# Performance work log

Hardware: AMD Instinct MI355X
Metric: run time of the kernel (lower is better)

## Reference

```python
import math
import jax, jax.numpy as jnp
import numpy as np

NUM_BUCKETS = 32
MAX_DISTANCE = 128
NUM_HEADS = 16


def _relative_position_bucket_bidirectional(relative_position):
    # encoder (is_decoder=False): split buckets for positive/negative, then log-spaced
    nb = NUM_BUCKETS // 2  # 16
    buckets = (relative_position > 0).astype(jnp.int32) * nb
    rp = jnp.abs(relative_position)
    max_exact = nb // 2  # 8
    is_small = rp < max_exact
    rp_safe = jnp.maximum(rp, 1)  # avoid log(0); masked out by is_small anyway
    large = max_exact + (
        jnp.log(rp_safe.astype(jnp.float32) / max_exact)
        / math.log(MAX_DISTANCE / max_exact)
        * (nb - max_exact)
    ).astype(jnp.int32)
    large = jnp.minimum(large, nb - 1)
    return buckets + jnp.where(is_small, rp, large)


def compute_bias(rel_bias, tgt_len, src_len):
    ctx = jnp.arange(tgt_len)[:, None]
    mem = jnp.arange(src_len)[None, :]
    buckets = _relative_position_bucket_bidirectional(mem - ctx)  # [T,S]
    values = rel_bias[buckets]            # [T,S,H]
    return jnp.transpose(values, (2, 0, 1))[None]  # [1,H,T,S]


def setup_inputs() -> dict:
    key = jax.random.key(0)
    ks = jax.random.split(key, 7)
    B, S, D = 4, 2048, 1024
    s = 1.0 / math.sqrt(D)
    return {
        "query_states": jax.random.normal(ks[0], (B, S, D), jnp.float32),
        "key_value_states": jax.random.normal(ks[1], (B, S, D), jnp.float32),
        "wq": jax.random.normal(ks[2], (D, D), jnp.float32) * s,
        "wk": jax.random.normal(ks[3], (D, D), jnp.float32) * s,
        "wv": jax.random.normal(ks[4], (D, D), jnp.float32) * s,
        "wo": jax.random.normal(ks[5], (D, D), jnp.float32) * s,
        "rel_bias": jax.random.normal(ks[6], (NUM_BUCKETS, NUM_HEADS), jnp.float32),
    }


def reference(query_states, key_value_states, wq, wk, wv, wo, rel_bias):
    B, T, D = query_states.shape
    S = key_value_states.shape[1]
    H = NUM_HEADS
    dh = D // H

    def shape(x, L):
        return jnp.transpose(x.reshape(B, L, H, dh), (0, 2, 1, 3))  # [B,H,L,dh]

    q = shape(query_states @ wq, T)
    k = shape(key_value_states @ wk, S)
    v = shape(key_value_states @ wv, S)

    bias = compute_bias(rel_bias, T, S)                      # [1,H,T,S]
    scores = jnp.einsum("bhtd,bhsd->bhts", q, k) + bias      # no 1/sqrt(d) scaling (T5)
    weights = jax.nn.softmax(scores, axis=-1)
    attn = jnp.einsum("bhts,bhsd->bhtd", weights, v)
    attn = jnp.transpose(attn, (0, 2, 1, 3)).reshape(B, T, D)
    return attn @ wo
```

## Files before the change

kernel.cpp:

```cpp
#include <hip/hip_runtime.h>
#include <hip/hip_bf16.h>
#include <math.h>

typedef __bf16 bf16;
typedef __attribute__((ext_vector_type(8))) __bf16 bf16x8;
typedef __attribute__((ext_vector_type(4))) __bf16 bf16x4;
typedef __attribute__((ext_vector_type(4))) float f32x4;
typedef __attribute__((ext_vector_type(16))) float f32x16;
typedef __attribute__((ext_vector_type(4), aligned(4))) float f32x4u;

#define B_  4
#define S_  2048
#define D_  1024
#define H_  16
#define DH_ 64
#define M_  (B_ * S_)
#define LOG2E 1.44269504088896f

static __device__ __forceinline__ f32x4 mfma16(bf16x8 a, bf16x8 b, f32x4 c) {
  return __builtin_amdgcn_mfma_f32_16x16x32_bf16(a, b, c, 0, 0, 0);
}
static __device__ __forceinline__ f32x16 mfma32(bf16x8 a, bf16x8 b, f32x16 c) {
  return __builtin_amdgcn_mfma_f32_32x32x16_bf16(a, b, c, 0, 0, 0);
}

static __device__ __forceinline__ void gld_lds16(const bf16* g, bf16* l) {
  __builtin_amdgcn_global_load_lds(
      (const __attribute__((address_space(1))) void*)g,
      (__attribute__((address_space(3))) void*)l, 16, 0, 0);
}

static __device__ __forceinline__ unsigned pkbf(float a, float b) {
  union { struct { __bf16 lo, hi; } s; unsigned u; } x;
  x.s.lo = (bf16)a; x.s.hi = (bf16)b;
  return x.u;
}

__global__ __launch_bounds__(256)
void cast2_kernel(const float* __restrict__ a, const float* __restrict__ bsrc,
                  bf16* __restrict__ oa, bf16* __restrict__ ob) {
  const int blk = blockIdx.x;
  const float* in = (blk < 8192) ? a : bsrc;
  bf16* out = (blk < 8192) ? oa : ob;
  size_t i = ((size_t)(blk & 8191) * 256 + threadIdx.x) * 4;
  float4 v = *(const float4*)(in + i);
  bf16x4 o = {(bf16)v.x, (bf16)v.y, (bf16)v.z, (bf16)v.w};
  *(bf16x4*)(out + i) = o;
}

__global__ __launch_bounds__(256)
void transpose_cast4_kernel(const float* __restrict__ w0, const float* __restrict__ w1,
                            const float* __restrict__ w2, const float* __restrict__ w3,
                            bf16* __restrict__ o0, bf16* __restrict__ o1,
                            bf16* __restrict__ o2, bf16* __restrict__ o3) {
  __shared__ float tile[32][33];
  const int z = blockIdx.z;
  const float* in = (z == 0) ? w0 : (z == 1) ? w1 : (z == 2) ? w2 : w3;
  bf16* out = (z == 0) ? o0 : (z == 1) ? o1 : (z == 2) ? o2 : o3;
  int n0 = blockIdx.x * 32, k0 = blockIdx.y * 32;
  int tx = threadIdx.x, ty = threadIdx.y;
#pragma unroll
  for (int j = 0; j < 32; j += 8)
    tile[ty + j][tx] = in[(size_t)(k0 + ty + j) * D_ + n0 + tx];
  __syncthreads();
#pragma unroll
  for (int j = 0; j < 32; j += 8)
    out[(size_t)(n0 + ty + j) * D_ + k0 + tx] = (bf16)tile[tx][ty + j];
}

__global__ __launch_bounds__(256)
void bias_table_kernel(const float* __restrict__ rel_bias, float* __restrict__ tab) {
  int i = blockIdx.x * 256 + threadIdx.x;
  int h = i >> 12, dp = i & 4095;
  int rel = dp - 2047;
  int bucket = (rel > 0) ? 16 : 0;
  int rp = rel < 0 ? -rel : rel;
  if (rp < 8) {
    bucket += rp;
  } else {
    int large = 8 + (int)(2.0f * __log2f((float)rp * 0.125f));
    bucket += (large < 15 ? large : 15);
  }
  tab[i] = rel_bias[bucket * H_ + h] * LOG2E - 64.0f;
}

__global__ __launch_bounds__(256)
void proj_gemm_kernel(const bf16* __restrict__ Xq, const bf16* __restrict__ Xkv,
                      const bf16* __restrict__ Wq, const bf16* __restrict__ Wk,
                      const bf16* __restrict__ Wv,
                      bf16* __restrict__ Qb, bf16* __restrict__ Kb, bf16* __restrict__ Vt) {
  const int K = D_;
  __shared__ bf16 As[128][64];
  __shared__ bf16 Bs[128][64];
  const int bid = blockIdx.x;
  const int xcd = bid & 7, j = bid >> 3;
  const int bx = j & 7;
  const int p = (j >> 3) + xcd * 24;
  const int by = p & 63, z = p >> 6;
  const bf16* A  = (z == 0) ? Xq : Xkv;
  const bf16* Bt = (z == 0) ? Wq : (z == 1) ? Wk : Wv;
  const int tid = threadIdx.x;
  const int brow = by * 128, bcol = bx * 128;
  const int wave = tid >> 6, lane = tid & 63;
  const int wr = (wave >> 1) * 64, wc = (wave & 1) * 64;
  const int lrow = lane & 15, lgrp = lane >> 4;

  f32x4 acc[4][4] = {};

  const int srow8 = tid >> 3;
  const int scol = ((tid & 7) ^ (srow8 & 7)) * 8;
  const bf16* ag = A + (size_t)(brow + srow8) * K + scol;
  const bf16* bg = Bt + (size_t)(bcol + srow8) * K + scol;
  const size_t r32 = (size_t)32 * K;
  bf16* al = &As[0][0] + tid * 8;
  bf16* bl = &Bs[0][0] + tid * 8;

  const int rsw = (lrow & 7) << 4;
  const char* arp = (const char*)&As[0][0];
  const char* brp = (const char*)&Bs[0][0];

  for (int k0 = 0; k0 < K; k0 += 64) {
    __syncthreads();
    gld_lds16(ag + k0,           al);
    gld_lds16(ag + k0 + r32,     al + 2048);
    gld_lds16(ag + k0 + 2 * r32, al + 4096);
    gld_lds16(ag + k0 + 3 * r32, al + 6144);
    gld_lds16(bg + k0,           bl);
    gld_lds16(bg + k0 + r32,     bl + 2048);
    gld_lds16(bg + k0 + 2 * r32, bl + 4096);
    gld_lds16(bg + k0 + 3 * r32, bl + 6144);
    __syncthreads();
#pragma unroll
    for (int kk = 0; kk < 2; ++kk) {
      bf16x8 af[4], bfr[4];
#pragma unroll
      for (int i = 0; i < 4; ++i) {
        af[i]  = *(const bf16x8*)(arp + (wr + i * 16 + lrow) * 128 +
                                  ((kk * 64 + (lgrp << 4)) ^ rsw));
        bfr[i] = *(const bf16x8*)(brp + (wc + i * 16 + lrow) * 128 +
                                  ((kk * 64 + (lgrp << 4)) ^ rsw));
      }
#pragma unroll
      for (int mi = 0; mi < 4; ++mi)
#pragma unroll
        for (int ni = 0; ni < 4; ++ni)
          acc[mi][ni] = mfma16(af[mi], bfr[ni], acc[mi][ni]);
    }
  }

  const float scl = (z == 0) ? LOG2E : 1.0f;
#pragma unroll
  for (int mi = 0; mi < 4; ++mi) {
    const int rowb = brow + wr + mi * 16 + lgrp * 4;
#pragma unroll
    for (int ni = 0; ni < 4; ++ni) {
      const int col = bcol + wc + ni * 16 + lrow;
      const int hh = col >> 6, d = col & (DH_ - 1);
      if (z == 2) {
        const int bb = rowb >> 11, s = rowb & (S_ - 1);
        bf16x4 pk = {(bf16)acc[mi][ni][0], (bf16)acc[mi][ni][1],
                     (bf16)acc[mi][ni][2], (bf16)acc[mi][ni][3]};
        *(bf16x4*)&Vt[((size_t)((bb * H_ + hh) * DH_ + d)) * S_ + s] = pk;
      } else {
#pragma unroll
        for (int r = 0; r < 4; ++r) {
          const float v = acc[mi][ni][r] * scl;
          const int m = rowb + r;
          const int bb = m >> 11, s = m & (S_ - 1);
          if (z == 0)
            Qb[((size_t)((bb * H_ + hh) * S_ + s)) * DH_ + d] = (bf16)v;
          else
            Kb[((size_t)((bb * H_ + hh) * S_ + s)) * DH_ + d] = (bf16)v;
        }
      }
    }
  }
}

__global__ __launch_bounds__(256)
void gemm_out_kernel(const bf16* __restrict__ A, const bf16* __restrict__ Bt,
                     float* __restrict__ Cout) {
  const int K = D_, N = D_;
  __shared__ bf16 As[128][64];
  __shared__ bf16 Bs[128][64];
  const int bid = blockIdx.x;
  const int xcd = bid & 7, j = bid >> 3;
  const int bx = j & 7;
  const int by = (j >> 3) + xcd * 8;
  const int tid = threadIdx.x;
  const int brow = by * 128, bcol = bx * 128;
  const int wave = tid >> 6, lane = tid & 63;
  const int wr = (wave >> 1) * 64, wc = (wave & 1) * 64;
  const int lrow = lane & 15, lgrp = lane >> 4;

  f32x4 acc[4][4] = {};

  const int srow8 = tid >> 3;
  const int scol = ((tid & 7) ^ (srow8 & 7)) * 8;
  const bf16* ag = A + (size_t)(brow + srow8) * K + scol;
  const bf16* bg = Bt + (size_t)(bcol + srow8) * K + scol;
  const size_t r32 = (size_t)32 * K;
  bf16* al = &As[0][0] + tid * 8;
  bf16* bl = &Bs[0][0] + tid * 8;

  const int rsw = (lrow & 7) << 4;
  const char* arp = (const char*)&As[0][0];
  const char* brp = (const char*)&Bs[0][0];

  for (int k0 = 0; k0 < K; k0 += 64) {
    __syncthreads();
    gld_lds16(ag + k0,           al);
    gld_lds16(ag + k0 + r32,     al + 2048);
    gld_lds16(ag + k0 + 2 * r32, al + 4096);
    gld_lds16(ag + k0 + 3 * r32, al + 6144);
    gld_lds16(bg + k0,           bl);
    gld_lds16(bg + k0 + r32,     bl + 2048);
    gld_lds16(bg + k0 + 2 * r32, bl + 4096);
    gld_lds16(bg + k0 + 3 * r32, bl + 6144);
    __syncthreads();
#pragma unroll
    for (int kk = 0; kk < 2; ++kk) {
      bf16x8 af[4], bfr[4];
#pragma unroll
      for (int i = 0; i < 4; ++i) {
        af[i]  = *(const bf16x8*)(arp + (wr + i * 16 + lrow) * 128 +
                                  ((kk * 64 + (lgrp << 4)) ^ rsw));
        bfr[i] = *(const bf16x8*)(brp + (wc + i * 16 + lrow) * 128 +
                                  ((kk * 64 + (lgrp << 4)) ^ rsw));
      }
#pragma unroll
      for (int mi = 0; mi < 4; ++mi)
#pragma unroll
        for (int ni = 0; ni < 4; ++ni)
          acc[mi][ni] = mfma16(af[mi], bfr[ni], acc[mi][ni]);
    }
  }

#pragma unroll
  for (int mi = 0; mi < 4; ++mi) {
    const int rowb = brow + wr + mi * 16 + lgrp * 4;
#pragma unroll
    for (int ni = 0; ni < 4; ++ni) {
      const int col = bcol + wc + ni * 16 + lrow;
#pragma unroll
      for (int r = 0; r < 4; ++r)
        Cout[(size_t)(rowb + r) * N + col] = acc[mi][ni][r];
    }
  }
}

__global__ __launch_bounds__(512, 4)
void attn_kernel(const bf16* __restrict__ Q, const bf16* __restrict__ Kb,
                 const bf16* __restrict__ Vt, const float* __restrict__ tab,
                 bf16* __restrict__ Oa) {
  __shared__ bf16 SB[4][4096];

  const int bid = blockIdx.x;
  const int w = ((bid & 7) << 6) + (bid >> 3);
  const int qt = w & 7, h = (w >> 3) & 15, b = w >> 7;
  const int tid = threadIdx.x;
  const int wave = tid >> 6, lane = tid & 63;
  const int l31 = lane & 31;
  const int hi = lane >> 5;
  const int t = qt * 256 + wave * 32 + l31;

  const bf16* Qp = Q + (size_t)(b * H_ + h) * S_ * DH_;
  const bf16* Kp = Kb + (size_t)(b * H_ + h) * S_ * DH_;
  const bf16* Vp = Vt + (size_t)(b * H_ + h) * DH_ * S_;
  const float* btb = tab + h * 4096 + 2047 - t;

  const int srow = tid >> 4;
  const int colS = (tid & 15) << 4;
  const int scol = colS ^ ((srow & 15) << 4);
  const bf16* ks0 = Kp + (size_t)(srow + 32 * (scol >> 7)) * DH_ + ((scol & 127) >> 1);
  const bf16* vs0 = Vp + (size_t)(srow + 32 * (scol >> 7)) * S_ + ((scol & 127) >> 1);
  bf16* sd = &SB[0][0] + tid * 8;

  const int swz = (l31 & 15) << 4;
  const char* rb = (const char*)&SB[0][0] + l31 * 256;
  const char* ra[4][2];
#pragma unroll
  for (int c = 0; c < 4; ++c)
#pragma unroll
    for (int sub = 0; sub < 2; ++sub)
      ra[c][sub] = rb + ((c * 32 + hi * 16 + sub * 128) ^ swz);

  bf16x8 qf[4];
#pragma unroll
  for (int c = 0; c < 4; ++c)
    qf[c] = *(const bf16x8*)&Qp[(size_t)t * DH_ + c * 16 + hi * 8];

  float l_r = 0.f;
  f32x16 o0 = {}, o1 = {};

  gld_lds16(ks0, sd);
  gld_lds16(vs0, sd + 8192);
  __syncthreads();

#define ATTN_TILE(BUF, S0)                                                        \
  {                                                                               \
    if ((S0) + 64 < S_) {                                                         \
      const int nb = (BUF) ^ 1;                                                   \
      gld_lds16(ks0 + (size_t)((S0) + 64) * DH_, sd + nb * 4096);                 \
      gld_lds16(vs0 + ((S0) + 64), sd + nb * 4096 + 8192);                        \
    }                                                                             \
    f32x16 sc0, sc1;                                                              \
    _Pragma("unroll")                                                             \
    for (int g = 0; g < 4; ++g) {                                                 \
      f32x4u b0 = *(const f32x4u*)(btb + (S0) + 8 * g + 4 * hi);                  \
      f32x4u b1 = *(const f32x4u*)(btb + (S0) + 32 + 8 * g + 4 * hi);             \
      _Pragma("unroll")                                                           \
      for (int v = 0; v < 4; ++v) { sc0[4 * g + v] = b0[v]; sc1[4 * g + v] = b1[v]; } \
    }                                                                             \
    _Pragma("unroll")                                                             \
    for (int c = 0; c < 4; ++c) {                                                 \
      bf16x8 k0 = *(const bf16x8*)(ra[c][0] + (BUF) * 8192);                      \
      bf16x8 k1 = *(const bf16x8*)(ra[c][1] + (BUF) * 8192);                      \
      sc0 = mfma32(k0, qf[c], sc0);                                               \
      sc1 = mfma32(k1, qf[c], sc1);                                               \
    }                                                                             \
    unsigned pw[16];                                                              \
    float q0s = 0.f, q1s = 0.f, q2s = 0.f, q3s = 0.f;                             \
    _Pragma("unroll")                                                             \
    for (int r2 = 0; r2 < 8; ++r2) {                                              \
      float a0 = __builtin_amdgcn_exp2f(sc0[2 * r2]);                             \
      float a1 = __builtin_amdgcn_exp2f(sc0[2 * r2 + 1]);                         \
      float c0 = __builtin_amdgcn_exp2f(sc1[2 * r2]);                             \
      float c1 = __builtin_amdgcn_exp2f(sc1[2 * r2 + 1]);                         \
      q0s += a0; q1s += a1; q2s += c0; q3s += c1;                                 \
      pw[r2] = pkbf(a0, a1);                                                      \
      pw[8 + r2] = pkbf(c0, c1);                                                  \
    }                                                                             \
    l_r += (q0s + q1s) + (q2s + q3s);                                             \
                 \
    unsigned sh[8];                                                               \
    _Pragma("unroll")                                                             \
    for (int g = 0; g < 4; ++g) {                                                 \
      const int base = (g & 1) * 4 + (g >> 1) * 8;                                \
      sh[2 * g]     = __shfl_xor(hi ? pw[base + 0] : pw[base + 2], 32);           \
      sh[2 * g + 1] = __shfl_xor(hi ? pw[base + 1] : pw[base + 3], 32);           \
    }                                                                             \
    _Pragma("unroll")                                                             \
    for (int g = 0; g < 4; ++g) {                                                 \
      const int base = (g & 1) * 4 + (g >> 1) * 8;                                \
      int4 bi = { (int)(hi ? sh[2 * g]     : pw[base + 0]),                       \
                  (int)(hi ? sh[2 * g + 1] : pw[base + 1]),                       \
                  (int)(hi ? pw[base + 2] : sh[2 * g]),                           \
                  (int)(hi ? pw[base + 3] : sh[2 * g + 1]) };                     \
      bf16x8 pb = *(bf16x8*)&bi;                                                  \
      bf16x8 v0 = *(const bf16x8*)(ra[g][0] + 16384 + (BUF) * 8192);              \
      bf16x8 v1 = *(const bf16x8*)(ra[g][1] + 16384 + (BUF) * 8192);              \
      o0 = mfma32(v0, pb, o0);                                                    \
      o1 = mfma32(v1, pb, o1);                                                    \
    }                                                                             \
    __syncthreads();                                                              \
  }

  for (int s0 = 0; s0 < S_; s0 += 128) {
    ATTN_TILE(0, s0)
    ATTN_TILE(1, s0 + 64)
  }
#undef ATTN_TILE

  l_r += __shfl_xor(l_r, 32);
  const float inv = 1.0f / l_r;
  bf16* Ob = Oa + ((size_t)(b * S_ + t)) * D_ + h * DH_;
#pragma unroll
  for (int g = 0; g < 4; ++g) {
    bf16x4 u0 = {(bf16)(o0[4 * g + 0] * inv), (bf16)(o0[4 * g + 1] * inv),
                 (bf16)(o0[4 * g + 2] * inv), (bf16)(o0[4 * g + 3] * inv)};
    *(bf16x4*)&Ob[8 * g + 4 * hi] = u0;
    bf16x4 u1 = {(bf16)(o1[4 * g + 0] * inv), (bf16)(o1[4 * g + 1] * inv),
                 (bf16)(o1[4 * g + 2] * inv), (bf16)(o1[4 * g + 3] * inv)};
    *(bf16x4*)&Ob[32 + 8 * g + 4 * hi] = u1;
  }
}

extern "C" void kernel_launch(void* const* d_in, const int* in_sizes, int n_in,
                              void* d_out, int out_size, void* d_ws, size_t ws_size,
                              hipStream_t stream) {
  const float* Xq   = (const float*)d_in[0];
  const float* Xkv  = (const float*)d_in[1];
  const float* Wq   = (const float*)d_in[2];
  const float* Wk   = (const float*)d_in[3];
  const float* Wv   = (const float*)d_in[4];
  const float* Wo   = (const float*)d_in[5];
  const float* relb = (const float*)d_in[6];
  float* out = (float*)d_out;

  char* ws = (char*)d_ws;
  const size_t SZ_X = (size_t)M_ * D_ * 2;
  const size_t SZ_W = (size_t)D_ * D_ * 2;
  bf16* Xq_b  = (bf16*)(ws);
  bf16* Xkv_b = (bf16*)(ws + SZ_X);
  bf16* Wq_t  = (bf16*)(ws + 2 * SZ_X);
  bf16* Wk_t  = (bf16*)(ws + 2 * SZ_X + SZ_W);
  bf16* Wv_t  = (bf16*)(ws + 2 * SZ_X + 2 * SZ_W);
  bf16* Wo_t  = (bf16*)(ws + 2 * SZ_X + 3 * SZ_W);
  bf16* Qb    = (bf16*)(ws + 2 * SZ_X + 4 * SZ_W);
  bf16* Kbuf  = (bf16*)(ws + 3 * SZ_X + 4 * SZ_W);
  bf16* Vt    = (bf16*)(ws + 4 * SZ_X + 4 * SZ_W);
  bf16* Ab    = (bf16*)(ws + 5 * SZ_X + 4 * SZ_W);
  float* tab  = (float*)(ws + 6 * SZ_X + 4 * SZ_W);

  cast2_kernel<<<16384, 256, 0, stream>>>(Xq, Xkv, Xq_b, Xkv_b);
  transpose_cast4_kernel<<<dim3(32, 32, 4), dim3(32, 8), 0, stream>>>(
      Wq, Wk, Wv, Wo, Wq_t, Wk_t, Wv_t, Wo_t);
  bias_table_kernel<<<256, 256, 0, stream>>>(relb, tab);

  proj_gemm_kernel<<<1536, 256, 0, stream>>>(
      Xq_b, Xkv_b, Wq_t, Wk_t, Wv_t, Qb, Kbuf, Vt);
  attn_kernel<<<512, 512, 0, stream>>>(Qb, Kbuf, Vt, tab, Ab);
  gemm_out_kernel<<<512, 256, 0, stream>>>(Ab, Wo_t, out);
}
```

Baseline: 205.5 us.

## Double-buffer LDS tiles in projection and output GEMMs with prefetch

Both GEMM kernels switch from a single 128x64 LDS tile per operand to two 128x32 buffers, with a 4-way XOR swizzle. The next K-slice is prefetched with global-to-LDS loads while the MFMAs run on the current buffer, which should overlap memory latency with compute. The cost is half as much work per sync (K-step of 32 instead of 64) and the same total LDS footprint, so each k-step does fewer MFMAs between barriers.

```diff
diff --git a/kernel.cpp b/kernel.cpp
--- a/kernel.cpp
+++ b/kernel.cpp
@@ -90,8 +90,8 @@
                       const bf16* __restrict__ Wv,
                       bf16* __restrict__ Qb, bf16* __restrict__ Kb, bf16* __restrict__ Vt) {
   const int K = D_;
-  __shared__ bf16 As[128][64];
-  __shared__ bf16 Bs[128][64];
+  __shared__ bf16 As[2][128][32];
+  __shared__ bf16 Bs[2][128][32];
   const int bid = blockIdx.x;
   const int xcd = bid & 7, j = bid >> 3;
   const int bx = j & 7;
@@ -107,46 +107,50 @@
 
   f32x4 acc[4][4] = {};
 
-  const int srow8 = tid >> 3;
-  const int scol = ((tid & 7) ^ (srow8 & 7)) * 8;
-  const bf16* ag = A + (size_t)(brow + srow8) * K + scol;
-  const bf16* bg = Bt + (size_t)(bcol + srow8) * K + scol;
-  const size_t r32 = (size_t)32 * K;
-  bf16* al = &As[0][0] + tid * 8;
-  bf16* bl = &Bs[0][0] + tid * 8;
-
-  const int rsw = (lrow & 7) << 4;
-  const char* arp = (const char*)&As[0][0];
-  const char* brp = (const char*)&Bs[0][0];
+  const int schunk = ((tid & 3) ^ ((tid >> 2) & 3)) * 8;
+  const bf16* ag = A + (size_t)(brow + (tid >> 2)) * K + schunk;
+  const bf16* bg = Bt + (size_t)(bcol + (tid >> 2)) * K + schunk;
+  const size_t rstep = (size_t)64 * K;
+  bf16* al = &As[0][0][0] + tid * 8;
+  bf16* bl = &Bs[0][0][0] + tid * 8;
+
+  const int rsw = (lrow & 3) << 4;
+  const char* arp = (const char*)&As[0][0][0];
+  const char* brp = (const char*)&Bs[0][0][0];
+
+  gld_lds16(ag, al);           gld_lds16(ag + rstep, al + 2048);
+  gld_lds16(bg, bl);           gld_lds16(bg + rstep, bl + 2048);
+  __syncthreads();
+
+#define PROJ_TILE(BUF, KO)                                                         \
+  {                                                                                \
+    if ((KO) + 32 < K) {                                                           \
+      gld_lds16(ag + (KO) + 32,         al + ((BUF) ^ 1) * 4096);                  \
+      gld_lds16(ag + (KO) + 32 + rstep, al + ((BUF) ^ 1) * 4096 + 2048);           \
+      gld_lds16(bg + (KO) + 32,         bl + ((BUF) ^ 1) * 4096);                  \
+      gld_lds16(bg + (KO) + 32 + rstep, bl + ((BUF) ^ 1) * 4096 + 2048);           \
+    }                                                                              \
+    bf16x8 af[4], bfr[4];                                                          \
+    _Pragma("unroll")                                                              \
+    for (int i = 0; i < 4; ++i) {                                                  \
+      af[i]  = *(const bf16x8*)(arp + (BUF) * 8192 +                               \
+                                (wr + i * 16 + lrow) * 64 + ((lgrp << 4) ^ rsw));  \
+      bfr[i] = *(const bf16x8*)(brp + (BUF) * 8192 +                               \
+                                (wc + i * 16 + lrow) * 64 + ((lgrp << 4) ^ rsw));  \
+    }                                                                              \
+    _Pragma("unroll")                                                              \
+    for (int mi = 0; mi < 4; ++mi)                                                 \
+      _Pragma("unroll")                                                            \
+      for (int ni = 0; ni < 4; ++ni)                                               \
+        acc[mi][ni] = mfma16(af[mi], bfr[ni], acc[mi][ni]);                        \
+    __syncthreads();                                                               \
+  }
 
   for (int k0 = 0; k0 < K; k0 += 64) {
-    __syncthreads();
-    gld_lds16(ag + k0,           al);
-    gld_lds16(ag + k0 + r32,     al + 2048);
-    gld_lds16(ag + k0 + 2 * r32, al + 4096);
-    gld_lds16(ag + k0 + 3 * r32, al + 6144);
-    gld_lds16(bg + k0,           bl);
-    gld_lds16(bg + k0 + r32,     bl + 2048);
-    gld_lds16(bg + k0 + 2 * r32, bl + 4096);
-    gld_lds16(bg + k0 + 3 * r32, bl + 6144);
-    __syncthreads();
-#pragma unroll
-    for (int kk = 0; kk < 2; ++kk) {
-      bf16x8 af[4], bfr[4];
-#pragma unroll
-      for (int i = 0; i < 4; ++i) {
-        af[i]  = *(const bf16x8*)(arp + (wr + i * 16 + lrow) * 128 +
-                                  ((kk * 64 + (lgrp << 4)) ^ rsw));
-        bfr[i] = *(const bf16x8*)(brp + (wc + i * 16 + lrow) * 128 +
-                                  ((kk * 64 + (lgrp << 4)) ^ rsw));
-      }
-#pragma unroll
-      for (int mi = 0; mi < 4; ++mi)
-#pragma unroll
-        for (int ni = 0; ni < 4; ++ni)
-          acc[mi][ni] = mfma16(af[mi], bfr[ni], acc[mi][ni]);
-    }
-  }
+    PROJ_TILE(0, k0)
+    PROJ_TILE(1, k0 + 32)
+  }
+#undef PROJ_TILE
 
   const float scl = (z == 0) ? LOG2E : 1.0f;
 #pragma unroll
@@ -181,8 +185,8 @@
 void gemm_out_kernel(const bf16* __restrict__ A, const bf16* __restrict__ Bt,
                      float* __restrict__ Cout) {
   const int K = D_, N = D_;
-  __shared__ bf16 As[128][64];
-  __shared__ bf16 Bs[128][64];
+  __shared__ bf16 As[2][128][32];
+  __shared__ bf16 Bs[2][128][32];
   const int bid = blockIdx.x;
   const int xcd = bid & 7, j = bid >> 3;
   const int bx = j & 7;
@@ -195,46 +199,50 @@
 
   f32x4 acc[4][4] = {};
 
-  const int srow8 = tid >> 3;
-  const int scol = ((tid & 7) ^ (srow8 & 7)) * 8;
-  const bf16* ag = A + (size_t)(brow + srow8) * K + scol;
-  const bf16* bg = Bt + (size_t)(bcol + srow8) * K + scol;
-  const size_t r32 = (size_t)32 * K;
-  bf16* al = &As[0][0] + tid * 8;
-  bf16* bl = &Bs[0][0] + tid * 8;
-
-  const int rsw = (lrow & 7) << 4;
-  const char* arp = (const char*)&As[0][0];
-  const char* brp = (const char*)&Bs[0][0];
+  const int schunk = ((tid & 3) ^ ((tid >> 2) & 3)) * 8;
+  const bf16* ag = A + (size_t)(brow + (tid >> 2)) * K + schunk;
+  const bf16* bg = Bt + (size_t)(bcol + (tid >> 2)) * K + schunk;
+  const size_t rstep = (size_t)64 * K;
+  bf16* al = &As[0][0][0] + tid * 8;
+  bf16* bl = &Bs[0][0][0] + tid * 8;
+
+  const int rsw = (lrow & 3) << 4;
+  const char* arp = (const char*)&As[0][0][0];
+  const char* brp = (const char*)&Bs[0][0][0];
+
+  gld_lds16(ag, al);           gld_lds16(ag + rstep, al + 2048);
+  gld_lds16(bg, bl);           gld_lds16(bg + rstep, bl + 2048);
+  __syncthreads();
+
+#define OUT_TILE(BUF, KO)                                                          \
+  {                                                                                \
+    if ((KO) + 32 < K) {                                                           \
+      gld_lds16(ag + (KO) + 32,         al + ((BUF) ^ 1) * 4096);                  \
+      gld_lds16(ag + (KO) + 32 + rstep, al + ((BUF) ^ 1) * 4096 + 2048);           \
+      gld_lds16(bg + (KO) + 32,         bl + ((BUF) ^ 1) * 4096);                  \
+      gld_lds16(bg + (KO) + 32 + rstep, bl + ((BUF) ^ 1) * 4096 + 2048);           \
+    }                                                                              \
+    bf16x8 af[4], bfr[4];                                                          \
+    _Pragma("unroll")                                                              \
+    for (int i = 0; i < 4; ++i) {                                                  \
+      af[i]  = *(const bf16x8*)(arp + (BUF) * 8192 +                               \
+                                (wr + i * 16 + lrow) * 64 + ((lgrp << 4) ^ rsw));  \
+      bfr[i] = *(const bf16x8*)(brp + (BUF) * 8192 +                               \
+                                (wc + i * 16 + lrow) * 64 + ((lgrp << 4) ^ rsw));  \
+    }                                                                              \
+    _Pragma("unroll")                                                              \
+    for (int mi = 0; mi < 4; ++mi)                                                 \
+      _Pragma("unroll")                                                            \
+      for (int ni = 0; ni < 4; ++ni)                                               \
+        acc[mi][ni] = mfma16(af[mi], bfr[ni], acc[mi][ni]);                        \
+    __syncthreads();                                                               \
+  }
 
   for (int k0 = 0; k0 < K; k0 += 64) {
-    __syncthreads();
-    gld_lds16(ag + k0,           al);
-    gld_lds16(ag + k0 + r32,     al + 2048);
-    gld_lds16(ag + k0 + 2 * r32, al + 4096);
-    gld_lds16(ag + k0 + 3 * r32, al + 6144);
-    gld_lds16(bg + k0,           bl);
-    gld_lds16(bg + k0 + r32,     bl + 2048);
-    gld_lds16(bg + k0 + 2 * r32, bl + 4096);
-    gld_lds16(bg + k0 + 3 * r32, bl + 6144);
-    __syncthreads();
-#pragma unroll
-    for (int kk = 0; kk < 2; ++kk) {
-      bf16x8 af[4], bfr[4];
-#pragma unroll
-      for (int i = 0; i < 4; ++i) {
-        af[i]  = *(const bf16x8*)(arp + (wr + i * 16 + lrow) * 128 +
-                                  ((kk * 64 + (lgrp << 4)) ^ rsw));
-        bfr[i] = *(const bf16x8*)(brp + (wc + i * 16 + lrow) * 128 +
-                                  ((kk * 64 + (lgrp << 4)) ^ rsw));
-      }
-#pragma unroll
-      for (int mi = 0; mi < 4; ++mi)
-#pragma unroll
-        for (int ni = 0; ni < 4; ++ni)
-          acc[mi][ni] = mfma16(af[mi], bfr[ni], acc[mi][ni]);
-    }
-  }
+    OUT_TILE(0, k0)
+    OUT_TILE(1, k0 + 32)
+  }
+#undef OUT_TILE
 
 #pragma unroll
   for (int mi = 0; mi < 4; ++mi) {
```

New measurement: 214.6 us. +4.4%, slower.
